# Performance work log

Hardware: AMD Instinct MI355X
Metric: run time of the kernel (lower is better)

The kernel has to match this reference:

```python
import jax, jax.numpy as jnp
import numpy as np

EPS = 1e-6


def _min_max_norm(v):
    # torch: 2.0 + (v - v.min()) / (v.max() - v.min()), global scalars
    mn, mx = v.min(), v.max()
    return 2.0 + (v - mn) / (mx - mn)


def setup_inputs() -> dict:
    key = jax.random.key(0)
    k1, k2, k3 = jax.random.split(key, 3)
    B, C, H, W = 2, 32, 96, 128
    return {
        "queries": jax.random.normal(k1, (B, C, H, W), jnp.float32),
        "keys": jax.random.normal(k2, (B, C, H, W), jnp.float32),
        "values": jax.random.normal(k3, (B, C, H, W), jnp.float32),
    }


def reference(queries, keys, values):
    B, C, H, W = queries.shape

    def row_column_softmax(s):  # s: [B,C,H,W]
        rc = jax.nn.softmax(s, axis=3) + jax.nn.softmax(s, axis=2)
        return rc / rc.max()

    def per_channel(q_c):  # q_c: [B,H,W] -> one output channel
        q = jnp.broadcast_to(q_c[:, None], (B, C, H, W))  # repeat over C
        # q_k_transpose: [B,C,H,H] (einsum sums w and y independently)
        hxh = jnp.einsum('bchw,bcxy->bchx', q, keys) + EPS
        # q_transpose_k: [B,C,W,W]
        wxw = jnp.einsum('bchw,bcxy->bcwy', q, keys) + EPS
        h_row = _min_max_norm(hxh.sum(axis=2))  # [B,C,H]  ('bcij->bcj')
        h_col = _min_max_norm(hxh.sum(axis=3))  # [B,C,H]  ('bcij->bci')
        w_row = _min_max_norm(wxw.sum(axis=2))  # [B,C,W]
        w_col = _min_max_norm(wxw.sum(axis=3))  # [B,C,W]
        outer = lambda m, n: jnp.einsum('bch,bcw->bchw', m, n)
        score = (row_column_softmax(outer(h_row, w_row))
                 + row_column_softmax(outer(h_row, w_col))
                 + row_column_softmax(outer(h_col, w_row))
                 + row_column_softmax(outer(h_col, w_col)))
        score = score / score.max()
        z_c = jnp.einsum('bchw,bchw->bhw', score, values)  # [B,H,W]
        return z_c, score

    # vectorize the original Python loop over query channels
    z_all, scores = jax.vmap(per_channel)(jnp.moveaxis(queries, 1, 0))
    z = jnp.swapaxes(z_all, 0, 1)  # [B,C,H,W]
    # torch returns the atten_score of the LAST loop iteration
    return z, scores[-1]
```

## Files before the change

kernel.cpp:

```cpp
#include <hip/hip_runtime.h>
#include <float.h>

#define BB 2
#define CC 32
#define HH 96
#define WW 128
#define HW (HH*WW)
#define BC (BB*CC)
#define NPLANE (BC*HW)
#define EPSF 1e-6f
#define LOG2E 1.4426950408889634f

#define QR_OFF 0
#define QC_OFF (QR_OFF + BC*HH)
#define QS_OFF (QC_OFF + BC*WW)
#define KR_OFF (QS_OFF + BC)
#define KC_OFF (KR_OFF + BC*HH)
#define KS_OFF (KC_OFF + BC*WW)
#define REC_OFF (KS_OFF + BC)
#define RECSZ 1344
#define BMX_OFF (REC_OFF + CC*BC*RECSZ)
#define BSX_OFF (BMX_OFF + CC*BC*4)

__device__ __forceinline__ float rcpf(float x) { return __builtin_amdgcn_rcpf(x); }
__device__ __forceinline__ float e2(float x) { return __builtin_amdgcn_exp2f(x); }

__device__ __forceinline__ float blkmax4(float v) {
  __shared__ float sred[4];
  #pragma unroll
  for (int o = 32; o > 0; o >>= 1) v = fmaxf(v, __shfl_xor(v, o, 64));
  if ((threadIdx.x & 63) == 0) sred[threadIdx.x >> 6] = v;
  __syncthreads();
  float r = fmaxf(fmaxf(sred[0], sred[1]), fmaxf(sred[2], sred[3]));
  __syncthreads();
  return r;
}

__global__ __launch_bounds__(256) void k1_plane_sums(const float* __restrict__ q,
                                                     const float* __restrict__ k,
                                                     float* __restrict__ ws) {
  int pb = blockIdx.x;
  int plane = pb & (BC - 1);
  const float* src = (pb < BC ? q : k) + (size_t)plane * HW;
  float* rowO = ws + (pb < BC ? QR_OFF : KR_OFF) + plane * HH;
  float* colO = ws + (pb < BC ? QC_OFF : KC_OFF) + plane * WW;
  float* totO = ws + (pb < BC ? QS_OFF : KS_OFF) + plane;
  __shared__ float cp[4 * WW];
  __shared__ float rsh[HH];
  __shared__ float wtot[2];
  int tid = threadIdx.x;
  int u = tid >> 6, l = tid & 63;
  float csum0 = 0.f, csum1 = 0.f;
  #pragma unroll 4
  for (int r = 0; r < 24; ++r) {
    int h = u * 24 + r;
    float v0 = src[h * WW + l];
    float v1 = src[h * WW + l + 64];
    csum0 += v0; csum1 += v1;
    float rs = v0 + v1;
    #pragma unroll
    for (int o = 1; o < 64; o <<= 1) rs += __shfl_xor(rs, o, 64);
    if (l == 0) { rowO[h] = rs; rsh[h] = rs; }
  }
  cp[u * WW + l] = csum0;
  cp[u * WW + l + 64] = csum1;
  __syncthreads();
  if (tid < WW) colO[tid] = cp[tid] + cp[WW + tid] + cp[2 * WW + tid] + cp[3 * WW + tid];
  float tv = (tid < HH) ? rsh[tid] : 0.f;
  if (tid < 128) {
    #pragma unroll
    for (int o = 1; o < 64; o <<= 1) tv += __shfl_xor(tv, o, 64);
    if ((tid & 63) == 0) wtot[tid >> 6] = tv;
  }
  __syncthreads();
  if (tid == 0) *totO = wtot[0] + wtot[1];
}

__device__ __forceinline__ float k2_raw(const float* __restrict__ ws, int type, int c0, int i, int L) {
  int bc = i / L, x = i - bc * L;
  int b = bc >> 5;
  if (type == 0) return ws[QS_OFF + b * CC + c0] * ws[KR_OFF + bc * HH + x] + HH * EPSF;
  if (type == 1) return ws[QR_OFF + (b * CC + c0) * HH + x] * ws[KS_OFF + bc] + HH * EPSF;
  if (type == 2) return ws[QS_OFF + b * CC + c0] * ws[KC_OFF + bc * WW + x] + WW * EPSF;
  return ws[QC_OFF + (b * CC + c0) * WW + x] * ws[KS_OFF + bc] + WW * EPSF;
}

__global__ __launch_bounds__(256) void k2_vec_norm(float* __restrict__ ws) {
  int c0 = blockIdx.x >> 2, type = blockIdx.x & 3;
  int L = (type < 2) ? HH : WW;
  int N = BC * L;
  int tid = threadIdx.x;
  float mx = -FLT_MAX, mn = FLT_MAX;
  for (int i = tid; i < N; i += 256) {
    float v = k2_raw(ws, type, c0, i, L);
    mx = fmaxf(mx, v); mn = fminf(mn, v);
  }
  mx = blkmax4(mx);
  mn = -blkmax4(-mn);
  float scale = rcpf(mx - mn);
  float fold = (type < 2) ? LOG2E : 1.0f;
  int fieldbase = (type == 0) ? 0 : (type == 1) ? 96 : (type == 2) ? 192 : 320;
  for (int i = tid; i < N; i += 256) {
    int bc = i / L, x = i - bc * L;
    float v = k2_raw(ws, type, c0, i, L);
    ws[REC_OFF + (size_t)(c0 * BC + bc) * RECSZ + fieldbase + x] =
        (2.0f + (v - mn) * scale) * fold;
  }
}

__global__ __launch_bounds__(256) void k3_rc(float* __restrict__ ws) {
  int vb = blockIdx.x;
  float* rec = ws + REC_OFF + (size_t)vb * RECSZ;
  int tid = threadIdx.x;
  int t = tid >> 6, l = tid & 63;
  __shared__ __align__(16) float mbuf[2 * HH];
  __shared__ __align__(16) float nbuf[2 * WW];
  __shared__ __align__(16) float rCs[4][WW];
  if (tid < 2 * HH) mbuf[tid] = rec[tid];
  nbuf[tid] = rec[192 + tid];
  __syncthreads();
  const float* mv = mbuf + (t >> 1) * 96;
  const float* nv = nbuf + (t & 1) * 128;
  float n0 = nv[l], n1 = nv[l + 64];
  float cs0 = 0.f, cs1 = 0.f;
  #pragma unroll 6
  for (int h = 0; h < HH; h += 4) {
    float4 mp = *(const float4*)&mv[h];
    cs0 += e2(mp.x * n0) + e2(mp.y * n0) + e2(mp.z * n0) + e2(mp.w * n0);
    cs1 += e2(mp.x * n1) + e2(mp.y * n1) + e2(mp.z * n1) + e2(mp.w * n1);
  }
  float rc0 = rcpf(cs0), rc1 = rcpf(cs1);
  rCs[t][l] = rc0; rCs[t][l + 64] = rc1;
  rec[832 + 4 * l + t] = rc0;
  rec[832 + 4 * (l + 64) + t] = rc1;
  int h0 = l >> 1, hf = l & 1;
  float m0 = mv[h0], m1 = mv[h0 + 32], m2 = mv[h0 + 64];
  const float* nb = nv + 64 * hf;
  float s0 = 0.f, s1 = 0.f, s2 = 0.f;
  #pragma unroll 4
  for (int j = 0; j < 64; j += 4) {
    float4 np = *(const float4*)&nb[j];
    s0 += e2(m0 * np.x) + e2(m0 * np.y) + e2(m0 * np.z) + e2(m0 * np.w);
    s1 += e2(m1 * np.x) + e2(m1 * np.y) + e2(m1 * np.z) + e2(m1 * np.w);
    s2 += e2(m2 * np.x) + e2(m2 * np.y) + e2(m2 * np.z) + e2(m2 * np.w);
  }
  s0 += __shfl_xor(s0, 1, 64);
  s1 += __shfl_xor(s1, 1, 64);
  s2 += __shfl_xor(s2, 1, 64);
  float rr0 = rcpf(s0), rr1 = rcpf(s1), rr2 = rcpf(s2);
  if (hf == 0) {
    rec[448 + 4 * h0 + t] = rr0;
    rec[448 + 4 * (h0 + 32) + t] = rr1;
    rec[448 + 4 * (h0 + 64) + t] = rr2;
  }
  const float* rcb = &rCs[t][64 * hf];
  float mx = 0.f;
  #pragma unroll 4
  for (int j = 0; j < 64; j += 4) {
    float4 np = *(const float4*)&nb[j];
    float4 rc = *(const float4*)&rcb[j];
    mx = fmaxf(mx, fmaxf(e2(m0 * np.x) * (rr0 + rc.x), e2(m0 * np.y) * (rr0 + rc.y)));
    mx = fmaxf(mx, fmaxf(e2(m0 * np.z) * (rr0 + rc.z), e2(m0 * np.w) * (rr0 + rc.w)));
    mx = fmaxf(mx, fmaxf(e2(m1 * np.x) * (rr1 + rc.x), e2(m1 * np.y) * (rr1 + rc.y)));
    mx = fmaxf(mx, fmaxf(e2(m1 * np.z) * (rr1 + rc.z), e2(m1 * np.w) * (rr1 + rc.w)));
    mx = fmaxf(mx, fmaxf(e2(m2 * np.x) * (rr2 + rc.x), e2(m2 * np.y) * (rr2 + rc.y)));
    mx = fmaxf(mx, fmaxf(e2(m2 * np.z) * (rr2 + rc.z), e2(m2 * np.w) * (rr2 + rc.w)));
  }
  #pragma unroll
  for (int o = 1; o < 64; o <<= 1) mx = fmaxf(mx, __shfl_xor(mx, o, 64));
  if (l == 0) ws[BMX_OFF + vb * 4 + t] = mx;
}

#define ELEMS 2
#define TILES 24
#define GRP 4
__global__ __launch_bounds__(256) void k4_score(const float* __restrict__ values,
                                                float* __restrict__ ws,
                                                float* __restrict__ out) {
  int bx = blockIdx.x;
  int tile = bx % TILES;
  int cb = bx / TILES;
  int b = cb & 1, c0 = cb >> 1;
  int tid = threadIdx.x;
  int base = tile * 512;
  int w = tid & 127;
  __shared__ __align__(16) float nS[GRP][256];
  __shared__ __align__(16) float c4S[GRP][512];
  __shared__ __align__(16) float mrf[CC * 24];
  __shared__ float s44[4][4];
  const float* rec0 = ws + REC_OFF + (size_t)(c0 * BC + b * CC) * RECSZ;
  float bm = ws[BMX_OFF + c0 * 256 + tid];
  #pragma unroll
  for (int o = 4; o <= 32; o <<= 1) bm = fmaxf(bm, __shfl_xor(bm, o, 64));
  if ((tid & 63) < 4) s44[tid >> 6][tid & 3] = bm;
  if (tid < 192) {
    int ch = tid / 6, f = tid - 6 * (tid / 6);
    const float* rsrc = rec0 + (size_t)ch * RECSZ;
    int soff = (f == 0) ? tile * 4 : (f == 1) ? 96 + tile * 4 : 448 + 16 * tile + 4 * (f - 2);
    *(float4*)&mrf[ch * 24 + f * 4] = *(const float4*)(rsrc + soff);
  }
  #pragma unroll
  for (int i = tid; i < GRP * 192; i += 256) {
    int chl = i / 192, rem = i - 192 * (i / 192);
    const float* rsrc = rec0 + (size_t)chl * RECSZ;
    float4 g4 = (rem < 64) ? *(const float4*)(rsrc + 192 + 4 * rem)
                           : *(const float4*)(rsrc + 832 + 4 * (rem - 64));
    if (rem < 64) *(float4*)&nS[chl][4 * rem] = g4;
    else          *(float4*)&c4S[chl][4 * (rem - 64)] = g4;
  }
  const float* vsrc0 = values + (size_t)(b * CC) * HW + base + tid;
  float v0 = vsrc0[0], v1 = vsrc0[256];
  __syncthreads();
  float im0 = rcpf(fmaxf(fmaxf(s44[0][0], s44[1][0]), fmaxf(s44[2][0], s44[3][0])));
  float im1 = rcpf(fmaxf(fmaxf(s44[0][1], s44[1][1]), fmaxf(s44[2][1], s44[3][1])));
  float im2 = rcpf(fmaxf(fmaxf(s44[0][2], s44[1][2]), fmaxf(s44[2][2], s44[3][2])));
  float im3 = rcpf(fmaxf(fmaxf(s44[0][3], s44[1][3]), fmaxf(s44[2][3], s44[3][3])));
  float* sbase = out + (size_t)NPLANE + (size_t)(b * CC) * HW + base + tid;
  bool writeS = (c0 == CC - 1);
  int r0 = tid >> 7;
  float U0 = 0.f, U1 = 0.f, smaxl = 0.f;
  for (int c = 0; c < CC; ++c) {
    if ((c & (GRP - 1)) == 0 && c) {
      __syncthreads();
      #pragma unroll
      for (int i = tid; i < GRP * 192; i += 256) {
        int chl = i / 192, rem = i - 192 * (i / 192);
        const float* rsrc = rec0 + (size_t)(c + chl) * RECSZ;
        float4 g4 = (rem < 64) ? *(const float4*)(rsrc + 192 + 4 * rem)
                               : *(const float4*)(rsrc + 832 + 4 * (rem - 64));
        if (rem < 64) *(float4*)&nS[chl][4 * rem] = g4;
        else          *(float4*)&c4S[chl][4 * (rem - 64)] = g4;
      }
      __syncthreads();
    }
    float nv0 = 0.f, nv1 = 0.f;
    if (c + 1 < CC) {
      nv0 = vsrc0[(size_t)(c + 1) * HW];
      nv1 = vsrc0[(size_t)(c + 1) * HW + 256];
    }
    int cl = c & (GRP - 1);
    float nr = nS[cl][w], nc = nS[cl][128 + w];
    float4 c4 = *(const float4*)&c4S[cl][4 * w];
    float A0 = c4.x * im0, A1 = c4.y * im1, A2 = c4.z * im2, A3 = c4.w * im3;
    const float* mc = &mrf[c * 24];
    #pragma unroll
    for (int j = 0; j < ELEMS; ++j) {
      int r = r0 + 2 * j;
      float mR = mc[r], mC = mc[4 + r];
      float4 r4 = *(const float4*)&mc[8 + 4 * r];
      float gx = fmaf(r4.x, im0, A0);
      float gy = fmaf(r4.y, im1, A1);
      float gz = fmaf(r4.z, im2, A2);
      float gw = fmaf(r4.w, im3, A3);
      float sc = e2(mR * nr) * gx + e2(mR * nc) * gy
               + e2(mC * nr) * gz + e2(mC * nc) * gw;
      smaxl = fmaxf(smaxl, sc);
      float uv = sc * (j == 0 ? v0 : v1);
      if (j == 0) U0 += uv; else U1 += uv;
      if (writeS) sbase[(size_t)c * HW + 256 * j] = sc;
    }
    v0 = nv0; v1 = nv1;
  }
  float* zout = out + (size_t)(b * CC + c0) * HW + base + tid;
  zout[0] = U0;
  zout[256] = U1;
  smaxl = blkmax4(smaxl);
  if (tid == 0) ws[BSX_OFF + bx] = smaxl;
}

__global__ __launch_bounds__(256) void k5_final(float* __restrict__ out,
                                                const float* __restrict__ ws) {
  int bx = blockIdx.x;
  int p = bx >> 3, sub = bx & 7;
  int c0 = p & (CC - 1);
  int tid = threadIdx.x;
  __shared__ float sm[2];
  if (tid < 64) {
    int l = tid;
    float a = (l < 48) ? ws[BSX_OFF + c0 * 48 + l] : 0.f;
    float c = (l < 48) ? ws[BSX_OFF + (CC - 1) * 48 + l] : 0.f;
    #pragma unroll
    for (int o = 1; o < 64; o <<= 1) {
      a = fmaxf(a, __shfl_xor(a, o, 64));
      c = fmaxf(c, __shfl_xor(c, o, 64));
    }
    if (l == 0) { sm[0] = a; sm[1] = c; }
  }
  __syncthreads();
  float ism = rcpf(sm[0]), isml = rcpf(sm[1]);
  int off = p * HW + sub * 1536 + tid;
  #pragma unroll
  for (int j = 0; j < 6; ++j) out[off + 256 * j] *= ism;
  #pragma unroll
  for (int j = 0; j < 6; ++j) out[NPLANE + off + 256 * j] *= isml;
}

extern "C" void kernel_launch(void* const* d_in, const int* in_sizes, int n_in,
                              void* d_out, int out_size, void* d_ws, size_t ws_size,
                              hipStream_t stream) {
  const float* q = (const float*)d_in[0];
  const float* k = (const float*)d_in[1];
  const float* v = (const float*)d_in[2];
  float* out = (float*)d_out;
  float* ws = (float*)d_ws;
  k1_plane_sums<<<2 * BC, 256, 0, stream>>>(q, k, ws);
  k2_vec_norm<<<CC * 4, 256, 0, stream>>>(ws);
  k3_rc<<<CC * BC, 256, 0, stream>>>(ws);
  k4_score<<<CC * BB * TILES, 256, 0, stream>>>(v, ws, out);
  k5_final<<<BC * 8, 256, 0, stream>>>(out, ws);
}
```

Measured before the change: 115.1 us.

## Split rc kernel into half-blocks and recompute last-channel score in final kernel

k3_rc now launches twice as many 128-thread blocks, each handling two of the four outer-product combinations, which raises parallelism and shrinks shared memory. The score-plane write is removed from k4_score, so the blocks that own the last channel no longer carry extra global stores that make them stragglers. k5_final gains 128 extra blocks that recompute the last channel's attention score from the per-plane records and write it already normalised, so the separate read-modify-write pass over that plane is dropped. This trades a small amount of recomputed exponentials for less memory traffic and better load balance in k4.

```diff
diff --git a/kernel.cpp b/kernel.cpp
--- a/kernel.cpp
+++ b/kernel.cpp
@@ -108,19 +108,19 @@
   }
 }
 
-__global__ __launch_bounds__(256) void k3_rc(float* __restrict__ ws) {
-  int vb = blockIdx.x;
+__global__ __launch_bounds__(128) void k3_rc(float* __restrict__ ws) {
+  int g = blockIdx.x;
+  int vb = g >> 1, pair = g & 1;
   float* rec = ws + REC_OFF + (size_t)vb * RECSZ;
   int tid = threadIdx.x;
-  int t = tid >> 6, l = tid & 63;
-  __shared__ __align__(16) float mbuf[2 * HH];
-  __shared__ __align__(16) float nbuf[2 * WW];
-  __shared__ __align__(16) float rCs[4][WW];
-  if (tid < 2 * HH) mbuf[tid] = rec[tid];
-  nbuf[tid] = rec[192 + tid];
-  __syncthreads();
-  const float* mv = mbuf + (t >> 1) * 96;
-  const float* nv = nbuf + (t & 1) * 128;
+  int u = tid >> 6, l = tid & 63;
+  int t = pair * 2 + u;
+  __shared__ __align__(16) float mn[448];
+  __shared__ float rCl[2][WW];
+  for (int i = tid; i < 112; i += 128) ((float4*)mn)[i] = ((const float4*)rec)[i];
+  __syncthreads();
+  const float* mv = mn + pair * 96;
+  const float* nv = mn + 192 + u * 128;
   float n0 = nv[l], n1 = nv[l + 64];
   float cs0 = 0.f, cs1 = 0.f;
   #pragma unroll 6
@@ -130,7 +130,7 @@
     cs1 += e2(mp.x * n1) + e2(mp.y * n1) + e2(mp.z * n1) + e2(mp.w * n1);
   }
   float rc0 = rcpf(cs0), rc1 = rcpf(cs1);
-  rCs[t][l] = rc0; rCs[t][l + 64] = rc1;
+  rCl[u][l] = rc0; rCl[u][l + 64] = rc1;
   rec[832 + 4 * l + t] = rc0;
   rec[832 + 4 * (l + 64) + t] = rc1;
   int h0 = l >> 1, hf = l & 1;
@@ -153,7 +153,8 @@
     rec[448 + 4 * (h0 + 32) + t] = rr1;
     rec[448 + 4 * (h0 + 64) + t] = rr2;
   }
-  const float* rcb = &rCs[t][64 * hf];
+  __syncthreads();
+  const float* rcb = &rCl[u][64 * hf];
   float mx = 0.f;
   #pragma unroll 4
   for (int j = 0; j < 64; j += 4) {
@@ -215,8 +216,6 @@
   float im1 = rcpf(fmaxf(fmaxf(s44[0][1], s44[1][1]), fmaxf(s44[2][1], s44[3][1])));
   float im2 = rcpf(fmaxf(fmaxf(s44[0][2], s44[1][2]), fmaxf(s44[2][2], s44[3][2])));
   float im3 = rcpf(fmaxf(fmaxf(s44[0][3], s44[1][3]), fmaxf(s44[2][3], s44[3][3])));
-  float* sbase = out + (size_t)NPLANE + (size_t)(b * CC) * HW + base + tid;
-  bool writeS = (c0 == CC - 1);
   int r0 = tid >> 7;
   float U0 = 0.f, U1 = 0.f, smaxl = 0.f;
   for (int c = 0; c < CC; ++c) {
@@ -257,7 +256,6 @@
       smaxl = fmaxf(smaxl, sc);
       float uv = sc * (j == 0 ? v0 : v1);
       if (j == 0) U0 += uv; else U1 += uv;
-      if (writeS) sbase[(size_t)c * HW + 256 * j] = sc;
     }
     v0 = nv0; v1 = nv1;
   }
@@ -268,31 +266,65 @@
   if (tid == 0) ws[BSX_OFF + bx] = smaxl;
 }
 
+#define K5_ZB (BC * 8)
 __global__ __launch_bounds__(256) void k5_final(float* __restrict__ out,
                                                 const float* __restrict__ ws) {
   int bx = blockIdx.x;
-  int p = bx >> 3, sub = bx & 7;
-  int c0 = p & (CC - 1);
-  int tid = threadIdx.x;
-  __shared__ float sm[2];
-  if (tid < 64) {
-    int l = tid;
-    float a = (l < 48) ? ws[BSX_OFF + c0 * 48 + l] : 0.f;
-    float c = (l < 48) ? ws[BSX_OFF + (CC - 1) * 48 + l] : 0.f;
-    #pragma unroll
-    for (int o = 1; o < 64; o <<= 1) {
-      a = fmaxf(a, __shfl_xor(a, o, 64));
-      c = fmaxf(c, __shfl_xor(c, o, 64));
-    }
-    if (l == 0) { sm[0] = a; sm[1] = c; }
-  }
-  __syncthreads();
-  float ism = rcpf(sm[0]), isml = rcpf(sm[1]);
-  int off = p * HW + sub * 1536 + tid;
-  #pragma unroll
-  for (int j = 0; j < 6; ++j) out[off + 256 * j] *= ism;
-  #pragma unroll
-  for (int j = 0; j < 6; ++j) out[NPLANE + off + 256 * j] *= isml;
+  int tid = threadIdx.x;
+  if (bx < K5_ZB) {
+    int p = bx >> 3, sub = bx & 7;
+    int c0 = p & (CC - 1);
+    __shared__ float sm;
+    if (tid < 64) {
+      float a = (tid < 48) ? ws[BSX_OFF + c0 * 48 + tid] : 0.f;
+      #pragma unroll
+      for (int o = 1; o < 64; o <<= 1) a = fmaxf(a, __shfl_xor(a, o, 64));
+      if (tid == 0) sm = a;
+    }
+    __syncthreads();
+    float ism = rcpf(sm);
+    int off = p * HW + sub * 1536 + tid;
+    #pragma unroll
+    for (int j = 0; j < 6; ++j) out[off + 256 * j] *= ism;
+  } else {
+    int sp = bx - K5_ZB;
+    int plane = sp >> 1, half = sp & 1;
+    const float* rec = ws + REC_OFF + (size_t)((CC - 1) * BC + plane) * RECSZ;
+    __shared__ __align__(16) float R[RECSZ];
+    __shared__ float s44[4][4];
+    __shared__ float sm;
+    for (int i = tid; i < RECSZ / 4; i += 256) ((float4*)R)[i] = ((const float4*)rec)[i];
+    float bm = ws[BMX_OFF + (CC - 1) * 256 + tid];
+    #pragma unroll
+    for (int o = 4; o <= 32; o <<= 1) bm = fmaxf(bm, __shfl_xor(bm, o, 64));
+    if ((tid & 63) < 4) s44[tid >> 6][tid & 3] = bm;
+    if (tid < 64) {
+      float a = (tid < 48) ? ws[BSX_OFF + (CC - 1) * 48 + tid] : 0.f;
+      #pragma unroll
+      for (int o = 1; o < 64; o <<= 1) a = fmaxf(a, __shfl_xor(a, o, 64));
+      if (tid == 0) sm = a;
+    }
+    __syncthreads();
+    float im0 = rcpf(fmaxf(fmaxf(s44[0][0], s44[1][0]), fmaxf(s44[2][0], s44[3][0])));
+    float im1 = rcpf(fmaxf(fmaxf(s44[0][1], s44[1][1]), fmaxf(s44[2][1], s44[3][1])));
+    float im2 = rcpf(fmaxf(fmaxf(s44[0][2], s44[1][2]), fmaxf(s44[2][2], s44[3][2])));
+    float im3 = rcpf(fmaxf(fmaxf(s44[0][3], s44[1][3]), fmaxf(s44[2][3], s44[3][3])));
+    float isml = rcpf(sm);
+    float* sout = out + (size_t)NPLANE + (size_t)plane * HW + half * 6144;
+    #pragma unroll 4
+    for (int e = tid; e < 6144; e += 256) {
+      int idx = half * 6144 + e;
+      int h = idx >> 7, ww = idx & 127;
+      float mR = R[h], mC = R[96 + h];
+      float nr = R[192 + ww], nc = R[320 + ww];
+      float4 r4 = *(const float4*)&R[448 + 4 * h];
+      float4 c4 = *(const float4*)&R[832 + 4 * ww];
+      float A0 = c4.x * im0, A1 = c4.y * im1, A2 = c4.z * im2, A3 = c4.w * im3;
+      float sc = e2(mR * nr) * fmaf(r4.x, im0, A0) + e2(mR * nc) * fmaf(r4.y, im1, A1)
+               + e2(mC * nr) * fmaf(r4.z, im2, A2) + e2(mC * nc) * fmaf(r4.w, im3, A3);
+      sout[e] = sc * isml;
+    }
+  }
 }
 
 extern "C" void kernel_launch(void* const* d_in, const int* in_sizes, int n_in,
@@ -305,7 +337,7 @@
   float* ws = (float*)d_ws;
   k1_plane_sums<<<2 * BC, 256, 0, stream>>>(q, k, ws);
   k2_vec_norm<<<CC * 4, 256, 0, stream>>>(ws);
-  k3_rc<<<CC * BC, 256, 0, stream>>>(ws);
+  k3_rc<<<CC * BC * 2, 128, 0, stream>>>(ws);
   k4_score<<<CC * BB * TILES, 256, 0, stream>>>(v, ws, out);
-  k5_final<<<BC * 8, 256, 0, stream>>>(out, ws);
-}
+  k5_final<<<K5_ZB + 128, 256, 0, stream>>>(out, ws);
+}
```

Measured after the change: 114.2 us. No clear change (-0.8%).
